# Kernel optimization log

Hardware: AMD Instinct MI355X
Metric: run time of the kernel (lower is better)

The kernel has to match this reference:

```python
import jax, jax.numpy as jnp
import numpy as np

EMBED_DIM = 256
NUM_HEADS = 8
HEAD_DIM = EMBED_DIM // NUM_HEADS
SCALING = HEAD_DIM ** -0.5
SEQ = 1024
BSZ = 4


def setup_inputs() -> dict:
    rng = jax.random.key(0)
    ks = jax.random.split(rng, 5)
    E = EMBED_DIM
    q = jax.random.normal(ks[0], (SEQ, BSZ, E), jnp.float32)
    k = jax.random.normal(ks[1], (SEQ, BSZ, E), jnp.float32)
    v = jax.random.normal(ks[2], (SEQ, BSZ, E), jnp.float32)
    # xavier-uniform-like scale for the packed 9E x E projection
    lim_in = np.sqrt(6.0 / (9 * E + E)).astype(np.float32)
    in_proj_w = jax.random.uniform(ks[3], (9 * E, E), jnp.float32, -lim_in, lim_in)
    in_proj_b = jnp.zeros((9 * E,), jnp.float32)
    lim_out = np.sqrt(6.0 / (E + E)).astype(np.float32)
    out_w = jax.random.uniform(ks[4], (E, E), jnp.float32, -lim_out, lim_out)
    out_b = jnp.zeros((E,), jnp.float32)
    return {"query": q, "key": k, "value": v,
            "in_proj_w": in_proj_w, "in_proj_b": in_proj_b,
            "out_w": out_w, "out_b": out_b,
            "shape0": 32, "shape1": 32}


def reference(query, key, value, in_proj_w, in_proj_b, out_w, out_b, shape0, shape1):
    S, B, E = query.shape
    H, hd = NUM_HEADS, HEAD_DIM

    def proj(x, i):  # slice i of the packed in-projection
        return x @ in_proj_w[i * E:(i + 1) * E].T + in_proj_b[i * E:(i + 1) * E]

    def heads(x):  # [S,B,E] -> [B*H, S, hd]
        return x.reshape(S, B * H, hd).transpose(1, 0, 2)

    q      = heads(proj(query, 0) * SCALING)
    k      = heads(proj(key, 1))
    v      = heads(proj(value, 2))
    q_left = heads(proj(query, 3))
    k_left = heads(proj(key, 4))
    q_right = heads(proj(query, 5))
    k_right = heads(proj(key, 6))
    q_loc  = heads(proj(query, 7) * SCALING)
    k_loc  = heads(proj(key, 8))

    global_w = q @ k.transpose(0, 2, 1)        # [BH,S,S]
    local_w  = q_loc @ k_loc.transpose(0, 2, 1)

    left_sm  = jax.nn.softmax(q_left @ k_left.transpose(0, 2, 1), axis=-1)
    right_sm = jax.nn.softmax(q_right @ k_right.transpose(0, 2, 1), axis=-1)

    triu = jnp.triu(jnp.ones((S, S), query.dtype))
    mini = jnp.tile(jnp.triu(jnp.ones((shape1, shape1), query.dtype)), (shape0, shape0))
    triu = (triu * mini)[None]                 # [1,S,S]
    triu_t = triu.transpose(0, 2, 1)

    fw_mask = (left_sm @ triu) * (right_sm @ triu_t)
    bw_mask = (left_sm @ triu_t) * (right_sm @ triu)
    local_mask = fw_mask + bw_mask             # [BH,S,S]

    attn_w = jax.nn.softmax(0.1 * global_w + local_w * local_mask, axis=-1)
    attn = (attn_w @ v).transpose(1, 0, 2).reshape(S, B, E)
    attn = attn @ out_w.T + out_b
    consistent_mask = local_mask.sum(axis=0)   # [S,S]
    return attn, consistent_mask
```

## Files before the change

### kernel.cpp

```cpp
#include <hip/hip_runtime.h>


typedef _Float16 v8h __attribute__((ext_vector_type(8)));
typedef _Float16 v4h __attribute__((ext_vector_type(4)));
typedef _Float16 v2h __attribute__((ext_vector_type(2)));
typedef float    v4f __attribute__((ext_vector_type(4)));

#define SL 1048576
#define RS 1032

static constexpr float SCALE = 0.17677669529663687f;
static constexpr float LOG2E = 1.4426950408889634f;


__global__ __launch_bounds__(256)
void cvt_kernel(const float* __restrict__ q, const float* __restrict__ k,
                const float* __restrict__ v, const float* __restrict__ W,
                _Float16* __restrict__ X16, _Float16* __restrict__ W16)
{
    const int b = blockIdx.x;
    const int t = threadIdx.x;
    const float* src; _Float16* dst; int off;
    if (b < 512)       { src = q; dst = X16;             off = b; }
    else if (b < 1024) { src = k; dst = X16 + (1 << 20); off = b - 512; }
    else if (b < 1536) { src = v; dst = X16 + (2 << 20); off = b - 1024; }
    else               { src = W; dst = W16;             off = b - 1536; }
    const int i = off * 2048 + t * 8;
    const float4 a = *(const float4*)(src + i);
    const float4 c = *(const float4*)(src + i + 4);
    v8h h;
    h[0] = (_Float16)a.x; h[1] = (_Float16)a.y; h[2] = (_Float16)a.z; h[3] = (_Float16)a.w;
    h[4] = (_Float16)c.x; h[5] = (_Float16)c.y; h[6] = (_Float16)c.z; h[7] = (_Float16)c.w;
    *(v8h*)(dst + i) = h;
}

__global__ __launch_bounds__(256)
void proj_kernel(const _Float16* __restrict__ X16, const _Float16* __restrict__ W16,
                 const float* __restrict__ bias, _Float16* __restrict__ P)
{
    __shared__ __align__(16) _Float16 stage[8192];
    const int t   = threadIdx.x;
    const int swz = (blockIdx.x & 7) * 144 + (blockIdx.x >> 3);
    const int n0  = (swz % 18) * 128;
    const int m0  = (swz / 18) * 64;
    const int slice = n0 >> 8;
    const int q4 = (n0 >> 7) & 1;
    const bool kslice = (slice == 1) || (slice == 4) || (slice == 6) || (slice == 8);
    const _Float16* X = X16 + (slice == 2 ? (2 << 20) : (kslice ? (1 << 20) : 0));
    const int w = t >> 6, lane = t & 63, m16 = lane & 15, kg = lane >> 4;
    const v4f zero = {0.f, 0.f, 0.f, 0.f};
    v4f acc[8] = {zero, zero, zero, zero, zero, zero, zero, zero};
    const _Float16* Arow = X + (size_t)(m0 + w * 16 + m16) * 256 + kg * 8;
    const _Float16* B0   = W16 + (size_t)(n0 + m16) * 256 + kg * 8;
#pragma unroll
    for (int kk = 0; kk < 8; ++kk) {
        const v8h a = *(const v8h*)(Arow + kk * 32);
#pragma unroll
        for (int nf = 0; nf < 8; ++nf) {
            const v8h bb = *(const v8h*)(B0 + nf * 4096 + kk * 32);
            acc[nf] = __builtin_amdgcn_mfma_f32_16x16x32_f16(a, bb, acc[nf], 0, 0, 0);
        }
    }
    const float scale = (slice == 0 || slice == 7) ? SCALE * LOG2E
                      : (slice == 3 || slice == 5) ? LOG2E : 1.0f;
#pragma unroll
    for (int nf = 0; nf < 8; ++nf) {
        const int c = n0 + nf * 16 + m16;
        const float bv = bias[c];
#pragma unroll
        for (int i = 0; i < 4; ++i) {
            const _Float16 val = (_Float16)((acc[nf][i] + bv) * scale);
            const int lb = i * 4 + (nf >> 1);
            int inner;
            if (slice == 2) {
                const int ls = w * 4 + kg;
                inner = ((nf & 1) << 8) + ((ls >> 3) << 7) + m16 * 8 + (ls & 7);
            } else {
                inner = ((w * 4 + kg) + (((nf & 1) * 2 + (m16 >> 3)) << 4)) * 8 + (m16 & 7);
            }
            stage[lb * 512 + inner] = val;
        }
    }
    __syncthreads();
    {
        const int o  = t * 32;
        const int lb = o >> 9;
        const int inner = o & 511;
        const int bs = lb >> 2, hh = lb & 3;
        const int bh = bs * 8 + q4 * 4 + hh;
        size_t dst;
        if (slice == 2) {
            const int kc = m0 >> 7;
            const int g0 = (m0 >> 5) & 3;
            const int nt = inner >> 8, a2 = (inner >> 7) & 1, r = inner & 127;
            dst = (size_t)2 * SL + (size_t)bh * 32768
                + (size_t)(kc * 1024 + nt * 512 + (g0 + a2) * 128 + r);
        } else {
            const int tile = m0 >> 6;
            dst = (size_t)slice * SL + (size_t)bh * 32768 + (size_t)(tile * 512 + inner);
        }
#pragma unroll
        for (int h8 = 0; h8 < 4; ++h8)
            *(v8h*)(P + dst + h8 * 8) = *(const v8h*)(stage + o + h8 * 8);
    }
}

__global__ __launch_bounds__(512, 4)
void attn_kernel(const _Float16* __restrict__ P, float* __restrict__ attn_pre,
                 _Float16* __restrict__ pmask)
{
    __shared__ __align__(16) _Float16 Lh[16 * RS];
    __shared__ __align__(16) _Float16 Rh[16 * RS];
    __shared__ __align__(16) _Float16 Ledge[16][36];
    __shared__ __align__(16) _Float16 Redge[16][36];
    __shared__ float Zp[8][16];

    const int t    = threadIdx.x;
    const int bid  = blockIdx.x;
    const int q    = bid >> 3;
    const int bh   = ((bid & 7) << 2) + (q & 3);
    const int rt   = q >> 2;
    const int w    = __builtin_amdgcn_readfirstlane(t >> 6);
    const int lane = t & 63;
    const int m16  = lane & 15;
    const int kg   = lane >> 4;

    const _Float16* Pb = P + (size_t)bh * 32768;
    const v4f zero = {0.f, 0.f, 0.f, 0.f};

    {
        const v8h a_l = *(const v8h*)(Pb + 3 * SL + rt * 512 + lane * 8);
        const v8h a_r = *(const v8h*)(Pb + 5 * SL + rt * 512 + lane * 8);
        const _Float16* Bl = Pb + 4 * SL;
        const _Float16* Br = Pb + 6 * SL;
#pragma unroll 4
        for (int jt2 = 0; jt2 < 8; ++jt2) {
            const int jt = (w << 3) + jt2;
            const v8h bL = *(const v8h*)(Bl + jt * 512 + lane * 8);
            const v8h bR = *(const v8h*)(Br + jt * 512 + lane * 8);
            v4f cL = __builtin_amdgcn_mfma_f32_16x16x32_f16(bL, a_l, zero, 0, 0, 0);
            v4f cR = __builtin_amdgcn_mfma_f32_16x16x32_f16(bR, a_r, zero, 0, 0, 0);
            v4h hL, hR;
#pragma unroll
            for (int i = 0; i < 4; ++i) { hL[i] = (_Float16)cL[i]; hR[i] = (_Float16)cR[i]; }
            const int base = m16 * RS + (jt << 4) + (kg << 2);
            *(v4h*)&Lh[base] = hL;
            *(v4h*)&Rh[base] = hR;
        }
    }
    __syncthreads();

    {
        const int kr = lane & 31;
        const int row0 = w << 1;
        _Float16* R0 = (lane >= 32) ? &Rh[row0 * RS] : &Lh[row0 * RS];
        _Float16* R1 = (lane >= 32) ? &Rh[(row0 + 1) * RS] : &Lh[(row0 + 1) * RS];
        _Float16* E0 = (lane >= 32) ? &Redge[row0][0] : &Ledge[row0][0];
        _Float16* E1 = (lane >= 32) ? &Redge[row0 + 1][0] : &Ledge[row0 + 1][0];
        v2h x[32];
        float t0 = 0.f, t1 = 0.f;
#pragma unroll
        for (int kb = 0; kb < 32; ++kb) {
            v2h pr;
            pr[0] = R0[(kb << 5) + kr];
            pr[1] = R1[(kb << 5) + kr];
            x[kb] = pr;
            t0 += __builtin_amdgcn_exp2f((float)pr[0]);
            t1 += __builtin_amdgcn_exp2f((float)pr[1]);
        }
#pragma unroll
        for (int off = 1; off < 32; off <<= 1) {
            t0 += __shfl_xor(t0, off, 32);
            t1 += __shfl_xor(t1, off, 32);
        }
        const float inv0 = 1.f / t0, inv1 = 1.f / t1;
#pragma unroll
        for (int kb = 0; kb < 32; ++kb) {
            v2h pr = x[kb];
            v2h nn;
            nn[0] = (_Float16)(__builtin_amdgcn_exp2f((float)pr[0]) * inv0);
            nn[1] = (_Float16)(__builtin_amdgcn_exp2f((float)pr[1]) * inv1);
            x[kb] = nn;
        }
#pragma unroll
        for (int kb = 0; kb < 32; ++kb) {
#pragma unroll
            for (int off = 1; off < 32; off <<= 1) {
                const int y = __shfl_up(__builtin_bit_cast(int, x[kb]), off, 32);
                if (kr >= off) x[kb] += __builtin_bit_cast(v2h, y);
            }
        }
#pragma unroll
        for (int kb = 1; kb < 32; ++kb) x[kb] += x[kb - 1];
#pragma unroll
        for (int kb = 0; kb < 32; ++kb) {
            R0[(kb << 5) + kr] = x[kb][0];
            R1[(kb << 5) + kr] = x[kb][1];
        }
        E0[kr + 1] = x[31][0];
        E1[kr + 1] = x[31][1];
        if (kr == 0) { E0[0] = (_Float16)0.f; E1[0] = (_Float16)0.f; }
    }
    __syncthreads();

    v4h p4[8];
    float psum = 0.f;
    {
        _Float16* pm = pmask + (size_t)bh * 1048576 + (size_t)rt * 16384;
        const v8h a_g = *(const v8h*)(Pb + 0 * SL + rt * 512 + lane * 8);
        const v8h a_c = *(const v8h*)(Pb + 7 * SL + rt * 512 + lane * 8);
        const _Float16* Bg = Pb + 1 * SL;
        const _Float16* Bc = Pb + 8 * SL;
        const int rr = m16 * RS;
#pragma unroll
        for (int jt2 = 0; jt2 < 8; ++jt2) {
            const int jt   = (w << 3) + jt2;
            const int jb   = jt >> 1;
            const int jr0  = ((jt & 1) << 4) + (kg << 2);
            const int colb = (jt << 4) + (kg << 2);
            const v8h bG = *(const v8h*)(Bg + jt * 512 + lane * 8);
            const v8h bC = *(const v8h*)(Bc + jt * 512 + lane * 8);
            const v4f g4 = __builtin_amdgcn_mfma_f32_16x16x32_f16(bG, a_g, zero, 0, 0, 0);
            const v4f l4 = __builtin_amdgcn_mfma_f32_16x16x32_f16(bC, a_c, zero, 0, 0, 0);
            const v4h PLv  = *(const v4h*)&Lh[rr + colb];
            const v4h PRv  = *(const v4h*)&Rh[rr + colb];
            const v4h eLcv = *(const v4h*)&Ledge[m16][jr0];
            const v4h eRcv = *(const v4h*)&Redge[m16][jr0];
            float eLb = 0.f, eRb = 0.f;
            if (jb) {
                eLb = (float)Lh[rr + (jb << 5) - 1];
                eRb = (float)Rh[rr + (jb << 5) - 1];
            }
            v4h m4;
#pragma unroll
            for (int i = 0; i < 4; ++i) {
                const int jrv = jr0 + i;
                const float PL  = (float)PLv[i];
                const float PR  = (float)PRv[i];
                const float eLc = (float)eLcv[i];
                const float eRc = (float)eRcv[i];
                float eLbc = 0.f, eRbc = 0.f;
                if (jb && jrv) {
                    const int o = rr + ((jb - 1) << 5) + jrv - 1;
                    eLbc = (float)Lh[o];
                    eRbc = (float)Rh[o];
                }
                const float SLv = 1.0f - eLb - eLc + eLbc;
                const float SRv = 1.0f - eRb - eRc + eRbc;
                const float mkv = PL * SRv + SLv * PR;
                const float pv  = __builtin_amdgcn_exp2f(0.1f * g4[i] + l4[i] * mkv);
                p4[jt2][i] = (_Float16)pv;
                psum += pv;
                m4[i] = (_Float16)mkv;
            }
            *(v4h*)(pm + ((size_t)jt << 8) + (m16 << 4) + (kg << 2)) = m4;
        }
        psum += __shfl_xor(psum, 16);
        psum += __shfl_xor(psum, 32);
        if (lane < 16) Zp[w][m16] = psum;
    }
    __syncthreads();

    {
#pragma unroll
        for (int jt2 = 0; jt2 < 8; ++jt2)
            *(v4h*)&Lh[m16 * RS + (((w << 3) + jt2) << 4) + (kg << 2)] = p4[jt2];
    }
    __syncthreads();

    {
        const int nt = w & 1, hf = w >> 1;
        v4f c = zero;
        const _Float16* Vb = Pb + 2 * SL + nt * 512 + lane * 8;
        const int kc0 = hf << 3;
#pragma unroll 4
        for (int kc2 = 0; kc2 < 8; ++kc2) {
            const int kc = kc0 + kc2;
            const v8h a = *(const v8h*)&Lh[m16 * RS + (kc << 5) + (kg << 3)];
            const v8h b = *(const v8h*)(Vb + (size_t)kc * 1024);
            c = __builtin_amdgcn_mfma_f32_16x16x32_f16(a, b, c, 0, 0, 0);
        }
        float* Pbuf = (float*)&Rh[0];
#pragma unroll
        for (int i = 0; i < 4; ++i) Pbuf[(w << 8) + (lane << 2) + i] = c[i];
    }
    __syncthreads();

    {
        const float* Pbuf = (const float*)&Rh[0];
        const int r   = t >> 5;
        const int d   = t & 31;
        const int nt2 = d >> 4, n = d & 15;
        const int kg2 = r >> 2, i2 = r & 3;
        const int off = (kg2 << 6) + (n << 2) + i2;
        float Z = 0.f;
#pragma unroll
        for (int w8 = 0; w8 < 8; ++w8) Z += Zp[w8][r];
        float v = 0.f;
#pragma unroll
        for (int hf = 0; hf < 4; ++hf)
            v += Pbuf[(((hf << 1) + nt2) << 8) + off];
        const int srow = (rt << 4) + r;
        attn_pre[((size_t)(srow * 4 + (bh >> 3))) * 256 + (bh & 7) * 32 + d] = v / Z;
    }
}

__global__ __launch_bounds__(256)
void tail_kernel(const _Float16* __restrict__ pmask, float* __restrict__ cmask,
                 const float* __restrict__ A, const float* __restrict__ W,
                 const float* __restrict__ bias, float* __restrict__ C)
{
    __shared__ __align__(16) float SMEM[4 * 16 * 136];
    const int bid = blockIdx.x;
    const int t = threadIdx.x;

    if (bid >= 256) {
        const int b2 = bid - 256;
        const int rt = b2 >> 3, wh = b2 & 7;
        float (*T4)[16][136] = (float(*)[16][136])SMEM;
        const int wv = t >> 6;
        const int lane = t & 63;
        float acc[8][4] = {};
        const _Float16* base = pmask + (size_t)rt * 16384 + ((size_t)wh << 11) + (lane << 2)
                             + ((size_t)wv << 3) * 1048576;
        for (int bh = 0; bh < 8; ++bh) {
            const _Float16* p = base + (size_t)bh * 1048576;
#pragma unroll
            for (int jt2 = 0; jt2 < 8; ++jt2) {
                const v4h h4 = *(const v4h*)(p + (jt2 << 8));
#pragma unroll
                for (int i = 0; i < 4; ++i) acc[jt2][i] += (float)h4[i];
            }
        }
#pragma unroll
        for (int jt2 = 0; jt2 < 8; ++jt2)
#pragma unroll
            for (int i = 0; i < 4; ++i)
                T4[wv][lane >> 2][(jt2 << 4) + ((lane & 3) << 2) + i] = acc[jt2][i];
        __syncthreads();
        const int row = t >> 4;
        const int c0  = (t & 15) << 3;
#pragma unroll
        for (int h = 0; h < 2; ++h) {
            const int c = c0 + (h << 2);
            const float4 s0 = *(const float4*)&T4[0][row][c];
            const float4 s1 = *(const float4*)&T4[1][row][c];
            const float4 s2 = *(const float4*)&T4[2][row][c];
            const float4 s3 = *(const float4*)&T4[3][row][c];
            const float4 o = make_float4(s0.x + s1.x + s2.x + s3.x,
                                         s0.y + s1.y + s2.y + s3.y,
                                         s0.z + s1.z + s2.z + s3.z,
                                         s0.w + s1.w + s2.w + s3.w);
            *(float4*)&cmask[((size_t)((rt << 4) + row) << 10) + (wh << 7) + c] = o;
        }
    } else {
        const int n0 = (bid & 3) * 64;
        const int m0 = (bid >> 2) * 64;
        float (*As)[68] = (float(*)[68])SMEM;
        float (*Bs)[68] = (float(*)[68])(SMEM + 16 * 68);
        const int tx = t & 15, ty = t >> 4;
        const int lm = t >> 2, lk = (t & 3) << 2;
        float acc[4][4] = {};
        for (int k0 = 0; k0 < 256; k0 += 16) {
            float4 av = *(const float4*)(A + (size_t)(m0 + lm) * 256 + k0 + lk);
            float4 bv = *(const float4*)(W + (size_t)(n0 + lm) * 256 + k0 + lk);
            As[lk + 0][lm] = av.x; As[lk + 1][lm] = av.y; As[lk + 2][lm] = av.z; As[lk + 3][lm] = av.w;
            Bs[lk + 0][lm] = bv.x; Bs[lk + 1][lm] = bv.y; Bs[lk + 2][lm] = bv.z; Bs[lk + 3][lm] = bv.w;
            __syncthreads();
#pragma unroll
            for (int kk = 0; kk < 16; ++kk) {
                float4 a4 = *(const float4*)&As[kk][ty << 2];
                float4 b4 = *(const float4*)&Bs[kk][tx << 2];
                float aa[4] = {a4.x, a4.y, a4.z, a4.w};
                float bb[4] = {b4.x, b4.y, b4.z, b4.w};
#pragma unroll
                for (int i = 0; i < 4; ++i)
#pragma unroll
                    for (int j = 0; j < 4; ++j)
                        acc[i][j] = fmaf(aa[i], bb[j], acc[i][j]);
            }
            __syncthreads();
        }
#pragma unroll
        for (int i = 0; i < 4; ++i) {
            const int m  = m0 + (ty << 2) + i;
            const int c0 = n0 + (tx << 2);
            float4 o = make_float4(acc[i][0] + bias[c0 + 0], acc[i][1] + bias[c0 + 1],
                                   acc[i][2] + bias[c0 + 2], acc[i][3] + bias[c0 + 3]);
            *(float4*)&C[(size_t)m * 256 + c0] = o;
        }
    }
}

extern "C" void kernel_launch(void* const* d_in, const int* in_sizes, int n_in,
                              void* d_out, int out_size, void* d_ws, size_t ws_size,
                              hipStream_t stream)
{
    const float* q  = (const float*)d_in[0];
    const float* k  = (const float*)d_in[1];
    const float* v  = (const float*)d_in[2];
    const float* Wi = (const float*)d_in[3];
    const float* bi = (const float*)d_in[4];
    const float* Wo = (const float*)d_in[5];
    const float* bo = (const float*)d_in[6];

    float* out      = (float*)d_out;
    float* attn_out = out;
    float* cmask    = out + 1048576;

    _Float16* Ppack    = (_Float16*)d_ws;
    float*    attn_pre = (float*)((char*)d_ws + 18874368);
    _Float16* pmask    = (_Float16*)((char*)d_ws + 23068672);
    _Float16* X16      = (_Float16*)((char*)d_ws + 90177536);
    _Float16* W16      = (_Float16*)((char*)d_ws + 96468992);

    cvt_kernel<<<1824, 256, 0, stream>>>(q, k, v, Wi, X16, W16);
    proj_kernel<<<1152, 256, 0, stream>>>(X16, W16, bi, Ppack);
    attn_kernel<<<2048, 512, 0, stream>>>(Ppack, attn_pre, pmask);
    tail_kernel<<<768, 256, 0, stream>>>(pmask, cmask, attn_pre, Wo, bo, attn_out);
}
```

Baseline: 236.3 us.

## Accumulate local mask over four heads per block in fp32 to cut mask traffic

```diff
diff --git a/kernel.cpp b/kernel.cpp
--- a/kernel.cpp
+++ b/kernel.cpp
@@ -107,7 +107,7 @@
 
 __global__ __launch_bounds__(512, 4)
 void attn_kernel(const _Float16* __restrict__ P, float* __restrict__ attn_pre,
-                 _Float16* __restrict__ pmask)
+                 float* __restrict__ pmask4)
 {
     __shared__ __align__(16) _Float16 Lh[16 * RS];
     __shared__ __align__(16) _Float16 Rh[16 * RS];
@@ -117,196 +117,207 @@
 
     const int t    = threadIdx.x;
     const int bid  = blockIdx.x;
-    const int q    = bid >> 3;
-    const int bh   = ((bid & 7) << 2) + (q & 3);
-    const int rt   = q >> 2;
+    const int xcd  = bid & 7;
+    const int rt   = bid >> 3;
     const int w    = __builtin_amdgcn_readfirstlane(t >> 6);
     const int lane = t & 63;
     const int m16  = lane & 15;
     const int kg   = lane >> 4;
 
-    const _Float16* Pb = P + (size_t)bh * 32768;
     const v4f zero = {0.f, 0.f, 0.f, 0.f};
-
-    {
-        const v8h a_l = *(const v8h*)(Pb + 3 * SL + rt * 512 + lane * 8);
-        const v8h a_r = *(const v8h*)(Pb + 5 * SL + rt * 512 + lane * 8);
-        const _Float16* Bl = Pb + 4 * SL;
-        const _Float16* Br = Pb + 6 * SL;
+    float* pm4 = pmask4 + ((size_t)xcd * 64 + rt) * 16384;
+
+#pragma unroll 1
+    for (int j = 0; j < 4; ++j) {
+        const int bh = (xcd << 2) + j;
+        const _Float16* Pb = P + (size_t)bh * 32768;
+
+        {
+            const v8h a_l = *(const v8h*)(Pb + 3 * SL + rt * 512 + lane * 8);
+            const v8h a_r = *(const v8h*)(Pb + 5 * SL + rt * 512 + lane * 8);
+            const _Float16* Bl = Pb + 4 * SL;
+            const _Float16* Br = Pb + 6 * SL;
 #pragma unroll 4
-        for (int jt2 = 0; jt2 < 8; ++jt2) {
-            const int jt = (w << 3) + jt2;
-            const v8h bL = *(const v8h*)(Bl + jt * 512 + lane * 8);
-            const v8h bR = *(const v8h*)(Br + jt * 512 + lane * 8);
-            v4f cL = __builtin_amdgcn_mfma_f32_16x16x32_f16(bL, a_l, zero, 0, 0, 0);
-            v4f cR = __builtin_amdgcn_mfma_f32_16x16x32_f16(bR, a_r, zero, 0, 0, 0);
-            v4h hL, hR;
-#pragma unroll
-            for (int i = 0; i < 4; ++i) { hL[i] = (_Float16)cL[i]; hR[i] = (_Float16)cR[i]; }
-            const int base = m16 * RS + (jt << 4) + (kg << 2);
-            *(v4h*)&Lh[base] = hL;
-            *(v4h*)&Rh[base] = hR;
-        }
-    }
-    __syncthreads();
-
-    {
-        const int kr = lane & 31;
-        const int row0 = w << 1;
-        _Float16* R0 = (lane >= 32) ? &Rh[row0 * RS] : &Lh[row0 * RS];
-        _Float16* R1 = (lane >= 32) ? &Rh[(row0 + 1) * RS] : &Lh[(row0 + 1) * RS];
-        _Float16* E0 = (lane >= 32) ? &Redge[row0][0] : &Ledge[row0][0];
-        _Float16* E1 = (lane >= 32) ? &Redge[row0 + 1][0] : &Ledge[row0 + 1][0];
-        v2h x[32];
-        float t0 = 0.f, t1 = 0.f;
-#pragma unroll
-        for (int kb = 0; kb < 32; ++kb) {
-            v2h pr;
-            pr[0] = R0[(kb << 5) + kr];
-            pr[1] = R1[(kb << 5) + kr];
-            x[kb] = pr;
-            t0 += __builtin_amdgcn_exp2f((float)pr[0]);
-            t1 += __builtin_amdgcn_exp2f((float)pr[1]);
-        }
-#pragma unroll
-        for (int off = 1; off < 32; off <<= 1) {
-            t0 += __shfl_xor(t0, off, 32);
-            t1 += __shfl_xor(t1, off, 32);
-        }
-        const float inv0 = 1.f / t0, inv1 = 1.f / t1;
-#pragma unroll
-        for (int kb = 0; kb < 32; ++kb) {
-            v2h pr = x[kb];
-            v2h nn;
-            nn[0] = (_Float16)(__builtin_amdgcn_exp2f((float)pr[0]) * inv0);
-            nn[1] = (_Float16)(__builtin_amdgcn_exp2f((float)pr[1]) * inv1);
-            x[kb] = nn;
-        }
-#pragma unroll
-        for (int kb = 0; kb < 32; ++kb) {
+            for (int jt2 = 0; jt2 < 8; ++jt2) {
+                const int jt = (w << 3) + jt2;
+                const v8h bL = *(const v8h*)(Bl + jt * 512 + lane * 8);
+                const v8h bR = *(const v8h*)(Br + jt * 512 + lane * 8);
+                v4f cL = __builtin_amdgcn_mfma_f32_16x16x32_f16(bL, a_l, zero, 0, 0, 0);
+                v4f cR = __builtin_amdgcn_mfma_f32_16x16x32_f16(bR, a_r, zero, 0, 0, 0);
+                v4h hL, hR;
+#pragma unroll
+                for (int i = 0; i < 4; ++i) { hL[i] = (_Float16)cL[i]; hR[i] = (_Float16)cR[i]; }
+                const int base = m16 * RS + (jt << 4) + (kg << 2);
+                *(v4h*)&Lh[base] = hL;
+                *(v4h*)&Rh[base] = hR;
+            }
+        }
+        __syncthreads();
+
+        {
+            const int kr = lane & 31;
+            const int row0 = w << 1;
+            _Float16* R0 = (lane >= 32) ? &Rh[row0 * RS] : &Lh[row0 * RS];
+            _Float16* R1 = (lane >= 32) ? &Rh[(row0 + 1) * RS] : &Lh[(row0 + 1) * RS];
+            _Float16* E0 = (lane >= 32) ? &Redge[row0][0] : &Ledge[row0][0];
+            _Float16* E1 = (lane >= 32) ? &Redge[row0 + 1][0] : &Ledge[row0 + 1][0];
+            v2h x[32];
+            float t0 = 0.f, t1 = 0.f;
+#pragma unroll
+            for (int kb = 0; kb < 32; ++kb) {
+                v2h pr;
+                pr[0] = R0[(kb << 5) + kr];
+                pr[1] = R1[(kb << 5) + kr];
+                x[kb] = pr;
+                t0 += __builtin_amdgcn_exp2f((float)pr[0]);
+                t1 += __builtin_amdgcn_exp2f((float)pr[1]);
+            }
 #pragma unroll
             for (int off = 1; off < 32; off <<= 1) {
-                const int y = __shfl_up(__builtin_bit_cast(int, x[kb]), off, 32);
-                if (kr >= off) x[kb] += __builtin_bit_cast(v2h, y);
-            }
-        }
-#pragma unroll
-        for (int kb = 1; kb < 32; ++kb) x[kb] += x[kb - 1];
-#pragma unroll
-        for (int kb = 0; kb < 32; ++kb) {
-            R0[(kb << 5) + kr] = x[kb][0];
-            R1[(kb << 5) + kr] = x[kb][1];
-        }
-        E0[kr + 1] = x[31][0];
-        E1[kr + 1] = x[31][1];
-        if (kr == 0) { E0[0] = (_Float16)0.f; E1[0] = (_Float16)0.f; }
-    }
-    __syncthreads();
-
-    v4h p4[8];
-    float psum = 0.f;
-    {
-        _Float16* pm = pmask + (size_t)bh * 1048576 + (size_t)rt * 16384;
-        const v8h a_g = *(const v8h*)(Pb + 0 * SL + rt * 512 + lane * 8);
-        const v8h a_c = *(const v8h*)(Pb + 7 * SL + rt * 512 + lane * 8);
-        const _Float16* Bg = Pb + 1 * SL;
-        const _Float16* Bc = Pb + 8 * SL;
-        const int rr = m16 * RS;
-#pragma unroll
-        for (int jt2 = 0; jt2 < 8; ++jt2) {
-            const int jt   = (w << 3) + jt2;
-            const int jb   = jt >> 1;
-            const int jr0  = ((jt & 1) << 4) + (kg << 2);
-            const int colb = (jt << 4) + (kg << 2);
-            const v8h bG = *(const v8h*)(Bg + jt * 512 + lane * 8);
-            const v8h bC = *(const v8h*)(Bc + jt * 512 + lane * 8);
-            const v4f g4 = __builtin_amdgcn_mfma_f32_16x16x32_f16(bG, a_g, zero, 0, 0, 0);
-            const v4f l4 = __builtin_amdgcn_mfma_f32_16x16x32_f16(bC, a_c, zero, 0, 0, 0);
-            const v4h PLv  = *(const v4h*)&Lh[rr + colb];
-            const v4h PRv  = *(const v4h*)&Rh[rr + colb];
-            const v4h eLcv = *(const v4h*)&Ledge[m16][jr0];
-            const v4h eRcv = *(const v4h*)&Redge[m16][jr0];
-            float eLb = 0.f, eRb = 0.f;
-            if (jb) {
-                eLb = (float)Lh[rr + (jb << 5) - 1];
-                eRb = (float)Rh[rr + (jb << 5) - 1];
-            }
-            v4h m4;
-#pragma unroll
-            for (int i = 0; i < 4; ++i) {
-                const int jrv = jr0 + i;
-                const float PL  = (float)PLv[i];
-                const float PR  = (float)PRv[i];
-                const float eLc = (float)eLcv[i];
-                const float eRc = (float)eRcv[i];
-                float eLbc = 0.f, eRbc = 0.f;
-                if (jb && jrv) {
-                    const int o = rr + ((jb - 1) << 5) + jrv - 1;
-                    eLbc = (float)Lh[o];
-                    eRbc = (float)Rh[o];
+                t0 += __shfl_xor(t0, off, 32);
+                t1 += __shfl_xor(t1, off, 32);
+            }
+            const float inv0 = 1.f / t0, inv1 = 1.f / t1;
+#pragma unroll
+            for (int kb = 0; kb < 32; ++kb) {
+                v2h pr = x[kb];
+                v2h nn;
+                nn[0] = (_Float16)(__builtin_amdgcn_exp2f((float)pr[0]) * inv0);
+                nn[1] = (_Float16)(__builtin_amdgcn_exp2f((float)pr[1]) * inv1);
+                x[kb] = nn;
+            }
+#pragma unroll
+            for (int kb = 0; kb < 32; ++kb) {
+#pragma unroll
+                for (int off = 1; off < 32; off <<= 1) {
+                    const int y = __shfl_up(__builtin_bit_cast(int, x[kb]), off, 32);
+                    if (kr >= off) x[kb] += __builtin_bit_cast(v2h, y);
                 }
-                const float SLv = 1.0f - eLb - eLc + eLbc;
-                const float SRv = 1.0f - eRb - eRc + eRbc;
-                const float mkv = PL * SRv + SLv * PR;
-                const float pv  = __builtin_amdgcn_exp2f(0.1f * g4[i] + l4[i] * mkv);
-                p4[jt2][i] = (_Float16)pv;
-                psum += pv;
-                m4[i] = (_Float16)mkv;
-            }
-            *(v4h*)(pm + ((size_t)jt << 8) + (m16 << 4) + (kg << 2)) = m4;
-        }
-        psum += __shfl_xor(psum, 16);
-        psum += __shfl_xor(psum, 32);
-        if (lane < 16) Zp[w][m16] = psum;
-    }
-    __syncthreads();
-
-    {
-#pragma unroll
-        for (int jt2 = 0; jt2 < 8; ++jt2)
-            *(v4h*)&Lh[m16 * RS + (((w << 3) + jt2) << 4) + (kg << 2)] = p4[jt2];
-    }
-    __syncthreads();
-
-    {
-        const int nt = w & 1, hf = w >> 1;
-        v4f c = zero;
-        const _Float16* Vb = Pb + 2 * SL + nt * 512 + lane * 8;
-        const int kc0 = hf << 3;
+            }
+#pragma unroll
+            for (int kb = 1; kb < 32; ++kb) x[kb] += x[kb - 1];
+#pragma unroll
+            for (int kb = 0; kb < 32; ++kb) {
+                R0[(kb << 5) + kr] = x[kb][0];
+                R1[(kb << 5) + kr] = x[kb][1];
+            }
+            E0[kr + 1] = x[31][0];
+            E1[kr + 1] = x[31][1];
+            if (kr == 0) { E0[0] = (_Float16)0.f; E1[0] = (_Float16)0.f; }
+        }
+        __syncthreads();
+
+        v4h p4[8];
+        float psum = 0.f;
+        {
+            const v8h a_g = *(const v8h*)(Pb + 0 * SL + rt * 512 + lane * 8);
+            const v8h a_c = *(const v8h*)(Pb + 7 * SL + rt * 512 + lane * 8);
+            const _Float16* Bg = Pb + 1 * SL;
+            const _Float16* Bc = Pb + 8 * SL;
+            const int rr = m16 * RS;
+#pragma unroll
+            for (int jt2 = 0; jt2 < 8; ++jt2) {
+                const int jt   = (w << 3) + jt2;
+                const int jb   = jt >> 1;
+                const int jr0  = ((jt & 1) << 4) + (kg << 2);
+                const int colb = (jt << 4) + (kg << 2);
+                const v8h bG = *(const v8h*)(Bg + jt * 512 + lane * 8);
+                const v8h bC = *(const v8h*)(Bc + jt * 512 + lane * 8);
+                const v4f g4 = __builtin_amdgcn_mfma_f32_16x16x32_f16(bG, a_g, zero, 0, 0, 0);
+                const v4f l4 = __builtin_amdgcn_mfma_f32_16x16x32_f16(bC, a_c, zero, 0, 0, 0);
+                const v4h PLv  = *(const v4h*)&Lh[rr + colb];
+                const v4h PRv  = *(const v4h*)&Rh[rr + colb];
+                const v4h eLcv = *(const v4h*)&Ledge[m16][jr0];
+                const v4h eRcv = *(const v4h*)&Redge[m16][jr0];
+                float eLb = 0.f, eRb = 0.f;
+                if (jb) {
+                    eLb = (float)Lh[rr + (jb << 5) - 1];
+                    eRb = (float)Rh[rr + (jb << 5) - 1];
+                }
+                v4f mk4;
+#pragma unroll
+                for (int i = 0; i < 4; ++i) {
+                    const int jrv = jr0 + i;
+                    const float PL  = (float)PLv[i];
+                    const float PR  = (float)PRv[i];
+                    const float eLc = (float)eLcv[i];
+                    const float eRc = (float)eRcv[i];
+                    float eLbc = 0.f, eRbc = 0.f;
+                    if (jb && jrv) {
+                        const int o = rr + ((jb - 1) << 5) + jrv - 1;
+                        eLbc = (float)Lh[o];
+                        eRbc = (float)Rh[o];
+                    }
+                    const float SLv = 1.0f - eLb - eLc + eLbc;
+                    const float SRv = 1.0f - eRb - eRc + eRbc;
+                    const float mkv = PL * SRv + SLv * PR;
+                    const float pv  = __builtin_amdgcn_exp2f(0.1f * g4[i] + l4[i] * mkv);
+                    p4[jt2][i] = (_Float16)pv;
+                    psum += pv;
+                    mk4[i] = mkv;
+                }
+                float* dst = pm4 + ((size_t)jt << 8) + (m16 << 4) + (kg << 2);
+                if (j == 0) {
+                    *(v4f*)dst = mk4;
+                } else {
+                    const v4f old = *(const v4f*)dst;
+                    *(v4f*)dst = old + mk4;
+                }
+            }
+            psum += __shfl_xor(psum, 16);
+            psum += __shfl_xor(psum, 32);
+            if (lane < 16) Zp[w][m16] = psum;
+        }
+        __syncthreads();
+
+        {
+#pragma unroll
+            for (int jt2 = 0; jt2 < 8; ++jt2)
+                *(v4h*)&Lh[m16 * RS + (((w << 3) + jt2) << 4) + (kg << 2)] = p4[jt2];
+        }
+        __syncthreads();
+
+        {
+            const int nt = w & 1, hf = w >> 1;
+            v4f c = zero;
+            const _Float16* Vb = Pb + 2 * SL + nt * 512 + lane * 8;
+            const int kc0 = hf << 3;
 #pragma unroll 4
-        for (int kc2 = 0; kc2 < 8; ++kc2) {
-            const int kc = kc0 + kc2;
-            const v8h a = *(const v8h*)&Lh[m16 * RS + (kc << 5) + (kg << 3)];
-            const v8h b = *(const v8h*)(Vb + (size_t)kc * 1024);
-            c = __builtin_amdgcn_mfma_f32_16x16x32_f16(a, b, c, 0, 0, 0);
-        }
-        float* Pbuf = (float*)&Rh[0];
-#pragma unroll
-        for (int i = 0; i < 4; ++i) Pbuf[(w << 8) + (lane << 2) + i] = c[i];
-    }
-    __syncthreads();
-
-    {
-        const float* Pbuf = (const float*)&Rh[0];
-        const int r   = t >> 5;
-        const int d   = t & 31;
-        const int nt2 = d >> 4, n = d & 15;
-        const int kg2 = r >> 2, i2 = r & 3;
-        const int off = (kg2 << 6) + (n << 2) + i2;
-        float Z = 0.f;
-#pragma unroll
-        for (int w8 = 0; w8 < 8; ++w8) Z += Zp[w8][r];
-        float v = 0.f;
-#pragma unroll
-        for (int hf = 0; hf < 4; ++hf)
-            v += Pbuf[(((hf << 1) + nt2) << 8) + off];
-        const int srow = (rt << 4) + r;
-        attn_pre[((size_t)(srow * 4 + (bh >> 3))) * 256 + (bh & 7) * 32 + d] = v / Z;
+            for (int kc2 = 0; kc2 < 8; ++kc2) {
+                const int kc = kc0 + kc2;
+                const v8h a = *(const v8h*)&Lh[m16 * RS + (kc << 5) + (kg << 3)];
+                const v8h b = *(const v8h*)(Vb + (size_t)kc * 1024);
+                c = __builtin_amdgcn_mfma_f32_16x16x32_f16(a, b, c, 0, 0, 0);
+            }
+            float* Pbuf = (float*)&Rh[0];
+#pragma unroll
+            for (int i = 0; i < 4; ++i) Pbuf[(w << 8) + (lane << 2) + i] = c[i];
+        }
+        __syncthreads();
+
+        {
+            const float* Pbuf = (const float*)&Rh[0];
+            const int r   = t >> 5;
+            const int d   = t & 31;
+            const int nt2 = d >> 4, n = d & 15;
+            const int kg2 = r >> 2, i2 = r & 3;
+            const int off = (kg2 << 6) + (n << 2) + i2;
+            float Z = 0.f;
+#pragma unroll
+            for (int w8 = 0; w8 < 8; ++w8) Z += Zp[w8][r];
+            float v = 0.f;
+#pragma unroll
+            for (int hf = 0; hf < 4; ++hf)
+                v += Pbuf[(((hf << 1) + nt2) << 8) + off];
+            const int srow = (rt << 4) + r;
+            attn_pre[((size_t)(srow * 4 + (bh >> 3))) * 256 + (bh & 7) * 32 + d] = v / Z;
+        }
+        if (j < 3) __syncthreads();
     }
 }
 
 __global__ __launch_bounds__(256)
-void tail_kernel(const _Float16* __restrict__ pmask, float* __restrict__ cmask,
+void tail_kernel(const float* __restrict__ pmask4, float* __restrict__ cmask,
                  const float* __restrict__ A, const float* __restrict__ W,
                  const float* __restrict__ bias, float* __restrict__ C)
 {
@@ -321,15 +332,16 @@
         const int wv = t >> 6;
         const int lane = t & 63;
         float acc[8][4] = {};
-        const _Float16* base = pmask + (size_t)rt * 16384 + ((size_t)wh << 11) + (lane << 2)
-                             + ((size_t)wv << 3) * 1048576;
-        for (int bh = 0; bh < 8; ++bh) {
-            const _Float16* p = base + (size_t)bh * 1048576;
+        const float* base = pmask4 + (size_t)rt * 16384 + ((size_t)wh << 11) + (lane << 2)
+                          + (size_t)(wv << 1) * 1048576;
+#pragma unroll
+        for (int g = 0; g < 2; ++g) {
+            const float* p = base + (size_t)g * 1048576;
 #pragma unroll
             for (int jt2 = 0; jt2 < 8; ++jt2) {
-                const v4h h4 = *(const v4h*)(p + (jt2 << 8));
-#pragma unroll
-                for (int i = 0; i < 4; ++i) acc[jt2][i] += (float)h4[i];
+                const float4 h4 = *(const float4*)(p + (jt2 << 8));
+                acc[jt2][0] += h4.x; acc[jt2][1] += h4.y;
+                acc[jt2][2] += h4.z; acc[jt2][3] += h4.w;
             }
         }
 #pragma unroll
@@ -410,12 +422,12 @@
 
     _Float16* Ppack    = (_Float16*)d_ws;
     float*    attn_pre = (float*)((char*)d_ws + 18874368);
-    _Float16* pmask    = (_Float16*)((char*)d_ws + 23068672);
+    float*    pmask4   = (float*)((char*)d_ws + 23068672);
     _Float16* X16      = (_Float16*)((char*)d_ws + 90177536);
     _Float16* W16      = (_Float16*)((char*)d_ws + 96468992);
 
     cvt_kernel<<<1824, 256, 0, stream>>>(q, k, v, Wi, X16, W16);
     proj_kernel<<<1152, 256, 0, stream>>>(X16, W16, bi, Ppack);
-    attn_kernel<<<2048, 512, 0, stream>>>(Ppack, attn_pre, pmask);
-    tail_kernel<<<768, 256, 0, stream>>>(pmask, cmask, attn_pre, Wo, bo, attn_out);
+    attn_kernel<<<512, 512, 0, stream>>>(Ppack, attn_pre, pmask4);
+    tail_kernel<<<768, 256, 0, stream>>>(pmask4, cmask, attn_pre, Wo, bo, attn_out);
 }
```

Measured after the change: 311.1 us. 1.32x slower.
